# Performance work log

Measured on AMD Instinct MI355X. Metric: run time of the kernel, lower is better.

Reference implementation:

```python
import jax, jax.numpy as jnp
import numpy as np

VOCAB, D, K, B, N = 100000, 512, 256, 4096, 8


def setup_inputs() -> dict:
    key = jax.random.key(0)
    ks = jax.random.split(key, 16)
    inp = {
        'subj_id': jax.random.randint(ks[0], (B, N), 0, VOCAB),
        'subj_w': jax.random.uniform(ks[1], (B, N), dtype=jnp.float32),
        'verb_id': jax.random.randint(ks[2], (B, N), 0, VOCAB),
        'verb_w': jax.random.uniform(ks[3], (B, N), dtype=jnp.float32),
        'obj_id': jax.random.randint(ks[4], (B, N), 0, VOCAB),
        'obj_w': jax.random.uniform(ks[5], (B, N), dtype=jnp.float32),
        'emb': jax.random.normal(ks[6], (VOCAB, D), dtype=jnp.float32) * 0.1,
        't1': jax.random.normal(ks[7], (K, D, D), dtype=jnp.float32) * 0.01,
        't2': jax.random.normal(ks[8], (K, D, D), dtype=jnp.float32) * 0.01,
        't3': jax.random.normal(ks[9], (K, K, K), dtype=jnp.float32) * 0.01,
        'W1': jax.random.normal(ks[10], (K, 2 * D), dtype=jnp.float32) * 0.02,
        'b1': jnp.zeros((K,), dtype=jnp.float32),
        'W2': jax.random.normal(ks[11], (K, 2 * D), dtype=jnp.float32) * 0.02,
        'b2': jnp.zeros((K,), dtype=jnp.float32),
        'W3': jax.random.normal(ks[12], (K, 2 * K), dtype=jnp.float32) * 0.02,
        'b3': jnp.zeros((K,), dtype=jnp.float32),
    }
    return inp


def _phrase_embed(emb, ids, w):
    # (B,N) ids, (B,N) weights -> (B,D) weighted sum of embeddings
    return jnp.einsum('bn,bnd->bd', w, emb[ids])


def _bilinear(t, a, b):
    # t: (k,n1,n2), a: (B,n1), b: (B,n2) -> (B,k)
    return jnp.einsum('kij,bi,bj->bk', t, a, b)


def reference(subj_id, subj_w, verb_id, verb_w, obj_id, obj_w,
              emb, t1, t2, t3, W1, b1, W2, b2, W3, b3):
    subj = _phrase_embed(emb, subj_id, subj_w)
    verb = _phrase_embed(emb, verb_id, verb_w)
    obj = _phrase_embed(emb, obj_id, obj_w)

    r1 = jnp.tanh(_bilinear(t1, subj, verb)
                  + jnp.concatenate([subj, verb], axis=1) @ W1.T + b1)
    r2 = jnp.tanh(_bilinear(t2, verb, obj)
                  + jnp.concatenate([verb, obj], axis=1) @ W2.T + b2)
    r3 = jnp.tanh(_bilinear(t3, r1, r2)
                  + jnp.concatenate([r1, r2], axis=1) @ W3.T + b3)
    return r3
```

## Files before the change

### kernel.cpp

```cpp
#include <hip/hip_runtime.h>
#include <hip/hip_bf16.h>
#include <stdint.h>

typedef __hip_bfloat16 bf16;
typedef __attribute__((ext_vector_type(4))) float f32x4;
typedef __attribute__((ext_vector_type(8))) short bf16x8;

#define K_DIM 256

__device__ __forceinline__ void gl2lds16(const void* g, void* l) {
  __builtin_amdgcn_global_load_lds(
      (const __attribute__((address_space(1))) unsigned int*)g,
      (__attribute__((address_space(3))) unsigned int*)l,
      16, 0, 0);
}

__global__ void embed_kernel(const int* __restrict__ sid, const float* __restrict__ sw,
                             const int* __restrict__ vid, const float* __restrict__ vw,
                             const int* __restrict__ oid, const float* __restrict__ ow,
                             const float* __restrict__ emb,
                             bf16* __restrict__ sv, bf16* __restrict__ vo) {
  int b = blockIdx.x;
  int t = threadIdx.x;
  float s0 = 0.f, s1 = 0.f, v0 = 0.f, v1 = 0.f, o0 = 0.f, o1 = 0.f;
#pragma unroll
  for (int n = 0; n < 8; ++n) {
    int i0 = b * 8 + n;
    { int id = sid[i0]; float w = sw[i0]; const float* r = emb + (size_t)id * 512; s0 += w * r[t]; s1 += w * r[t + 256]; }
    { int id = vid[i0]; float w = vw[i0]; const float* r = emb + (size_t)id * 512; v0 += w * r[t]; v1 += w * r[t + 256]; }
    { int id = oid[i0]; float w = ow[i0]; const float* r = emb + (size_t)id * 512; o0 += w * r[t]; o1 += w * r[t + 256]; }
  }
  size_t base = (size_t)b * 1024;
  bf16 vb0 = __float2bfloat16(v0), vb1 = __float2bfloat16(v1);
  sv[base + t]       = __float2bfloat16(s0);
  sv[base + 256 + t] = __float2bfloat16(s1);
  sv[base + 512 + t] = vb0;
  sv[base + 768 + t] = vb1;
  vo[base + t]       = vb0;
  vo[base + 256 + t] = vb1;
  vo[base + 512 + t] = __float2bfloat16(o0);
  vo[base + 768 + t] = __float2bfloat16(o1);
}

__global__ void cvt_kernel(const float* __restrict__ in, bf16* __restrict__ out, int n) {
  int i = blockIdx.x * blockDim.x + threadIdx.x;
  if (i < n) out[i] = __float2bfloat16(in[i]);
}

__global__ void tcvt_kernel(const float* __restrict__ in, bf16* __restrict__ out, int N) {
  __shared__ float tile[32][33];
  int k = blockIdx.z;
  size_t base = (size_t)k * N * N;
  int j0 = blockIdx.x * 32, i0 = blockIdx.y * 32;
  int tx = threadIdx.x, ty = threadIdx.y;
#pragma unroll
  for (int r = 0; r < 4; ++r)
    tile[ty + 8 * r][tx] = in[base + (size_t)(i0 + ty + 8 * r) * N + j0 + tx];
  __syncthreads();
#pragma unroll
  for (int r = 0; r < 4; ++r)
    out[base + (size_t)(j0 + ty + 8 * r) * N + i0 + tx] = __float2bfloat16(tile[tx][ty + 8 * r]);
}

__global__ __launch_bounds__(256) void lin_kernel(
    const bf16* __restrict__ A, const bf16* __restrict__ W,
    const float* __restrict__ bias, float* __restrict__ Lout, int inner) {
  __shared__ __align__(16) bf16 As[128 * 64];
  __shared__ __align__(16) bf16 Bs[64 * 64];
  int tid = threadIdx.x;
  int wv = tid >> 6, lane = tid & 63;
  int wr = wv >> 1, wc = wv & 1;
  int cl = lane & 15, rg = lane >> 4;
  int r8 = lane >> 3, c8 = lane & 7;
  int cs = c8 ^ r8;
  int b0 = blockIdx.x * 128;
  int n0 = blockIdx.y * 64;
  f32x4 acc[4][2] = {};
  int KO = inner >> 6;
  for (int ko = 0; ko < KO; ++ko) {
    __syncthreads();
#pragma unroll
    for (int it = 0; it < 4; ++it) {
      int m = wv * 32 + it * 8 + r8;
      gl2lds16(A + (size_t)(b0 + m) * inner + ko * 64 + cs * 8, &As[(wv * 32 + it * 8) * 64]);
    }
#pragma unroll
    for (int it = 0; it < 2; ++it) {
      int nn = wv * 16 + it * 8 + r8;
      gl2lds16(W + (size_t)(n0 + nn) * inner + ko * 64 + cs * 8, &Bs[(wv * 16 + it * 8) * 64]);
    }
    __syncthreads();
#pragma unroll
    for (int ks = 0; ks < 2; ++ks) {
      bf16x8 a[4], bb[2];
      int sw = (ks * 4 + rg) ^ (cl & 7);
#pragma unroll
      for (int mt = 0; mt < 4; ++mt) a[mt] = *(const bf16x8*)&As[(wr * 64 + mt * 16 + cl) * 64 + sw * 8];
#pragma unroll
      for (int nt = 0; nt < 2; ++nt) bb[nt] = *(const bf16x8*)&Bs[(wc * 32 + nt * 16 + cl) * 64 + sw * 8];
#pragma unroll
      for (int mt = 0; mt < 4; ++mt)
#pragma unroll
        for (int nt = 0; nt < 2; ++nt)
          acc[mt][nt] = __builtin_amdgcn_mfma_f32_16x16x32_bf16(a[mt], bb[nt], acc[mt][nt], 0, 0, 0);
    }
  }
#pragma unroll
  for (int mt = 0; mt < 4; ++mt)
#pragma unroll
    for (int nt = 0; nt < 2; ++nt) {
      int col = n0 + wc * 32 + nt * 16 + cl;
      float bv = bias[col];
#pragma unroll
      for (int r = 0; r < 4; ++r) {
        int row = b0 + wr * 64 + mt * 16 + rg * 4 + r;
        Lout[(size_t)row * K_DIM + col] = acc[mt][nt][r] + bv;
      }
    }
}

__global__ __launch_bounds__(256) void bilin_kernel(
    const bf16* __restrict__ A, int lda,
    const bf16* __restrict__ T,
    const bf16* __restrict__ V, int ldv, int voff,
    const float* __restrict__ Lm,
    int I, int J,
    bf16* __restrict__ outb, int ldo, int ooff,
    float* __restrict__ outf) {
  __shared__ __align__(16) bf16 As[128 * 64];
  __shared__ __align__(16) bf16 Bs[128 * 64];
  int tid = threadIdx.x;
  int wv = tid >> 6, lane = tid & 63;
  int wr = wv >> 1, wc = wv & 1;
  int cl = lane & 15, rg = lane >> 4;
  int r8 = lane >> 3, c8 = lane & 7;
  int cs = c8 ^ r8;
  int b0 = blockIdx.x * 128;
  int k = blockIdx.y;
  const bf16* Tk = T + (size_t)k * J * I;
  float rsum[16];
#pragma unroll
  for (int v = 0; v < 16; ++v) rsum[v] = 0.f;
  int KO = I >> 6, JB = J >> 7;
  for (int jb = 0; jb < JB; ++jb) {
    f32x4 acc[4][4] = {};
    for (int ko = 0; ko < KO; ++ko) {
      __syncthreads();
#pragma unroll
      for (int it = 0; it < 4; ++it) {
        int m = wv * 32 + it * 8 + r8;
        gl2lds16(A + (size_t)(b0 + m) * lda + ko * 64 + cs * 8, &As[(wv * 32 + it * 8) * 64]);
        gl2lds16(Tk + (size_t)(jb * 128 + m) * I + ko * 64 + cs * 8, &Bs[(wv * 32 + it * 8) * 64]);
      }
      __syncthreads();
#pragma unroll
      for (int ks = 0; ks < 2; ++ks) {
        bf16x8 a[4], bb[4];
        int sw = (ks * 4 + rg) ^ (cl & 7);
#pragma unroll
        for (int mt = 0; mt < 4; ++mt) a[mt] = *(const bf16x8*)&As[(wr * 64 + mt * 16 + cl) * 64 + sw * 8];
#pragma unroll
        for (int nt = 0; nt < 4; ++nt) bb[nt] = *(const bf16x8*)&Bs[(wc * 64 + nt * 16 + cl) * 64 + sw * 8];
#pragma unroll
        for (int mt = 0; mt < 4; ++mt)
#pragma unroll
          for (int nt = 0; nt < 4; ++nt)
            acc[mt][nt] = __builtin_amdgcn_mfma_f32_16x16x32_bf16(a[mt], bb[nt], acc[mt][nt], 0, 0, 0);
      }
    }
#pragma unroll
    for (int mt = 0; mt < 4; ++mt)
#pragma unroll
      for (int r = 0; r < 4; ++r) {
        int gb = b0 + wr * 64 + mt * 16 + rg * 4 + r;
        const bf16* vrow = V + (size_t)gb * ldv + voff + jb * 128 + wc * 64 + cl;
#pragma unroll
        for (int nt = 0; nt < 4; ++nt)
          rsum[mt * 4 + r] += acc[mt][nt][r] * __bfloat162float(vrow[nt * 16]);
      }
  }
#pragma unroll
  for (int v = 0; v < 16; ++v) {
    float x = rsum[v];
    x += __shfl_xor(x, 1);
    x += __shfl_xor(x, 2);
    x += __shfl_xor(x, 4);
    x += __shfl_xor(x, 8);
    rsum[v] = x;
  }
  float* rsum_s = (float*)As;
  __syncthreads();
  if (cl == 0) {
#pragma unroll
    for (int mt = 0; mt < 4; ++mt)
#pragma unroll
      for (int r = 0; r < 4; ++r)
        rsum_s[wc * 128 + wr * 64 + mt * 16 + rg * 4 + r] = rsum[mt * 4 + r];
  }
  __syncthreads();
  if (tid < 128) {
    int gb = b0 + tid;
    float s = rsum_s[tid] + rsum_s[128 + tid] + Lm[(size_t)gb * K_DIM + k];
    float t = tanhf(s);
    if (outb) outb[(size_t)gb * ldo + ooff + k] = __float2bfloat16(t);
    else outf[(size_t)gb * K_DIM + k] = t;
  }
}

extern "C" void kernel_launch(void* const* d_in, const int* in_sizes, int n_in,
                              void* d_out, int out_size, void* d_ws, size_t ws_size,
                              hipStream_t stream) {
  const int*   sid = (const int*)d_in[0];
  const float* sw  = (const float*)d_in[1];
  const int*   vid = (const int*)d_in[2];
  const float* vw  = (const float*)d_in[3];
  const int*   oid = (const int*)d_in[4];
  const float* ow  = (const float*)d_in[5];
  const float* emb = (const float*)d_in[6];
  const float* t1  = (const float*)d_in[7];
  const float* t2  = (const float*)d_in[8];
  const float* t3  = (const float*)d_in[9];
  const float* W1  = (const float*)d_in[10];
  const float* b1  = (const float*)d_in[11];
  const float* W2  = (const float*)d_in[12];
  const float* b2  = (const float*)d_in[13];
  const float* W3  = (const float*)d_in[14];
  const float* b3  = (const float*)d_in[15];

  char* ws = (char*)d_ws;
  bf16*  Tbuf = (bf16*)(ws);
  bf16*  W1b  = (bf16*)(ws + 134217728ull);
  bf16*  W2b  = (bf16*)(ws + 134742016ull);
  bf16*  W3b  = (bf16*)(ws + 135266304ull);
  bf16*  sv   = (bf16*)(ws + 135528448ull);
  bf16*  vo   = (bf16*)(ws + 143917056ull);
  float* Lb   = (float*)(ws + 152305664ull);
  bf16*  r12  = (bf16*)(ws + 156499968ull);

  embed_kernel<<<4096, 256, 0, stream>>>(sid, sw, vid, vw, oid, ow, emb, sv, vo);
  cvt_kernel<<<1024, 256, 0, stream>>>(W1, W1b, 256 * 1024);
  cvt_kernel<<<1024, 256, 0, stream>>>(W2, W2b, 256 * 1024);
  cvt_kernel<<<512, 256, 0, stream>>>(W3, W3b, 256 * 512);

  lin_kernel<<<dim3(32, 4), 256, 0, stream>>>(sv, W1b, b1, Lb, 1024);
  tcvt_kernel<<<dim3(16, 16, 256), dim3(32, 8), 0, stream>>>(t1, Tbuf, 512);
  bilin_kernel<<<dim3(32, 256), 256, 0, stream>>>(sv, 1024, Tbuf, sv, 1024, 512, Lb, 512, 512,
                                                  r12, 512, 0, nullptr);
  lin_kernel<<<dim3(32, 4), 256, 0, stream>>>(vo, W2b, b2, Lb, 1024);
  tcvt_kernel<<<dim3(16, 16, 256), dim3(32, 8), 0, stream>>>(t2, Tbuf, 512);
  bilin_kernel<<<dim3(32, 256), 256, 0, stream>>>(vo, 1024, Tbuf, vo, 1024, 512, Lb, 512, 512,
                                                  r12, 512, 256, nullptr);
  lin_kernel<<<dim3(32, 4), 256, 0, stream>>>(r12, W3b, b3, Lb, 512);
  tcvt_kernel<<<dim3(8, 8, 256), dim3(32, 8), 0, stream>>>(t3, Tbuf, 256);
  bilin_kernel<<<dim3(32, 256), 256, 0, stream>>>(r12, 512, Tbuf, r12, 512, 256, Lb, 256, 256,
                                                  nullptr, 0, 0, (float*)d_out);
}
```

Before: 3.904 ms.

## Use 256x256 tiles with double-buffered LDS prefetch in bilinear kernel

Rewrites the bilinear kernel to use 512-thread blocks that each compute a 256x256 tile, with double-buffered LDS so global-to-LDS loads for the next step run while MFMAs work on the current one. The jb/ko loops are flattened into one pipelined loop, and MFMA sections are raised with setprio. Partial contractions with V are accumulated in a shared scratch array. The larger tile cuts global loads per FLOP and hides load latency, at the cost of more LDS (about 130KB) and more registers, which lowers occupancy.

```diff
diff --git a/kernel.cpp b/kernel.cpp
--- a/kernel.cpp
+++ b/kernel.cpp
@@ -119,91 +119,120 @@
     }
 }
 
-__global__ __launch_bounds__(256) void bilin_kernel(
+__global__ __launch_bounds__(512) void bilin256_kernel(
     const bf16* __restrict__ A, int lda,
     const bf16* __restrict__ T,
     const bf16* __restrict__ V, int ldv, int voff,
     const float* __restrict__ Lm,
-    int I, int J,
+    int I, int J, int koshift,
     bf16* __restrict__ outb, int ldo, int ooff,
     float* __restrict__ outf) {
-  __shared__ __align__(16) bf16 As[128 * 64];
-  __shared__ __align__(16) bf16 Bs[128 * 64];
-  int tid = threadIdx.x;
-  int wv = tid >> 6, lane = tid & 63;
-  int wr = wv >> 1, wc = wv & 1;
-  int cl = lane & 15, rg = lane >> 4;
-  int r8 = lane >> 3, c8 = lane & 7;
-  int cs = c8 ^ r8;
-  int b0 = blockIdx.x * 128;
-  int k = blockIdx.y;
+  __shared__ __align__(16) bf16 As[2][256 * 64];
+  __shared__ __align__(16) bf16 Bs[2][256 * 64];
+  __shared__ float scratch[4][256];
+
+  const int tid  = threadIdx.x;
+  const int wv   = tid >> 6;
+  const int lane = tid & 63;
+  const int wr   = wv >> 2;
+  const int wc   = wv & 3;
+  const int cl   = lane & 15;
+  const int rg   = lane >> 4;
+  const int c8   = lane & 7;
+  const int r8   = lane >> 3;
+  const int cs   = c8 ^ r8;
+  const int b0   = blockIdx.x * 256;
+  const int k    = blockIdx.y;
   const bf16* Tk = T + (size_t)k * J * I;
-  float rsum[16];
-#pragma unroll
-  for (int v = 0; v < 16; ++v) rsum[v] = 0.f;
-  int KO = I >> 6, JB = J >> 7;
-  for (int jb = 0; jb < JB; ++jb) {
-    f32x4 acc[4][4] = {};
-    for (int ko = 0; ko < KO; ++ko) {
-      __syncthreads();
-#pragma unroll
-      for (int it = 0; it < 4; ++it) {
-        int m = wv * 32 + it * 8 + r8;
-        gl2lds16(A + (size_t)(b0 + m) * lda + ko * 64 + cs * 8, &As[(wv * 32 + it * 8) * 64]);
-        gl2lds16(Tk + (size_t)(jb * 128 + m) * I + ko * 64 + cs * 8, &Bs[(wv * 32 + it * 8) * 64]);
+  const int KOm  = (1 << koshift) - 1;
+  const int NT   = (J >> 8) << koshift;
+
+  auto stage_half = [&](int s, int q) {
+    const int db   = s & 1;
+    const int ko_s = s & KOm;
+    const int jb_s = s >> koshift;
+    const int hrow = (q & 1) * 128;
+#pragma unroll
+    for (int p = 0; p < 2; ++p) {
+      const int rloc = hrow + p * 64 + wv * 8 + r8;
+      if (q < 2)
+        gl2lds16(A + (size_t)(b0 + rloc) * lda + ko_s * 64 + cs * 8,
+                 &As[db][(hrow + p * 64 + wv * 8) * 64]);
+      else
+        gl2lds16(Tk + (size_t)(jb_s * 256 + rloc) * I + ko_s * 64 + cs * 8,
+                 &Bs[db][(hrow + p * 64 + wv * 8) * 64]);
+    }
+  };
+
+  const f32x4 zero4 = {0.f, 0.f, 0.f, 0.f};
+  f32x4 acc[8][4];
+
+#pragma unroll
+  for (int q = 0; q < 4; ++q) stage_half(0, q);
+
+  for (int t = 0; t < NT; ++t) {
+    __syncthreads();
+    const int db = t & 1;
+    const int ko = t & KOm;
+    const int jb = t >> koshift;
+    if (ko == 0) {
+#pragma unroll
+      for (int m = 0; m < 8; ++m)
+#pragma unroll
+        for (int n = 0; n < 4; ++n) acc[m][n] = zero4;
+    }
+    const int s = t + 1;
+    const bool hasNext = (s < NT);
+#pragma unroll
+    for (int ph = 0; ph < 2; ++ph) {
+      if (hasNext) { stage_half(s, ph * 2); stage_half(s, ph * 2 + 1); }
+      const int sw = (ph * 4 + rg) ^ c8;
+      bf16x8 a[8], bb[4];
+#pragma unroll
+      for (int mt = 0; mt < 8; ++mt)
+        a[mt] = *(const bf16x8*)&As[db][(wr * 128 + mt * 16 + cl) * 64 + sw * 8];
+#pragma unroll
+      for (int nt = 0; nt < 4; ++nt)
+        bb[nt] = *(const bf16x8*)&Bs[db][(wc * 64 + nt * 16 + cl) * 64 + sw * 8];
+      __builtin_amdgcn_s_setprio(1);
+#pragma unroll
+      for (int mt = 0; mt < 8; ++mt)
+#pragma unroll
+        for (int nt = 0; nt < 4; ++nt)
+          acc[mt][nt] = __builtin_amdgcn_mfma_f32_16x16x32_bf16(a[mt], bb[nt], acc[mt][nt], 0, 0, 0);
+      __builtin_amdgcn_s_setprio(0);
+    }
+    if (ko == KOm) {
+#pragma unroll
+      for (int m = 0; m < 8; ++m) {
+#pragma unroll
+        for (int r = 0; r < 4; ++r) {
+          const int row = wr * 128 + m * 16 + rg * 4 + r;
+          const bf16* vrow = V + (size_t)(b0 + row) * ldv + voff + jb * 256 + wc * 64 + cl;
+          float x = acc[m][0][r] * __bfloat162float(vrow[0])
+                  + acc[m][1][r] * __bfloat162float(vrow[16])
+                  + acc[m][2][r] * __bfloat162float(vrow[32])
+                  + acc[m][3][r] * __bfloat162float(vrow[48]);
+          x += __shfl_xor(x, 1);
+          x += __shfl_xor(x, 2);
+          x += __shfl_xor(x, 4);
+          x += __shfl_xor(x, 8);
+          if (cl == 0) {
+            if (jb == 0) scratch[wc][row] = x;
+            else         scratch[wc][row] += x;
+          }
+        }
       }
-      __syncthreads();
-#pragma unroll
-      for (int ks = 0; ks < 2; ++ks) {
-        bf16x8 a[4], bb[4];
-        int sw = (ks * 4 + rg) ^ (cl & 7);
-#pragma unroll
-        for (int mt = 0; mt < 4; ++mt) a[mt] = *(const bf16x8*)&As[(wr * 64 + mt * 16 + cl) * 64 + sw * 8];
-#pragma unroll
-        for (int nt = 0; nt < 4; ++nt) bb[nt] = *(const bf16x8*)&Bs[(wc * 64 + nt * 16 + cl) * 64 + sw * 8];
-#pragma unroll
-        for (int mt = 0; mt < 4; ++mt)
-#pragma unroll
-          for (int nt = 0; nt < 4; ++nt)
-            acc[mt][nt] = __builtin_amdgcn_mfma_f32_16x16x32_bf16(a[mt], bb[nt], acc[mt][nt], 0, 0, 0);
-      }
-    }
-#pragma unroll
-    for (int mt = 0; mt < 4; ++mt)
-#pragma unroll
-      for (int r = 0; r < 4; ++r) {
-        int gb = b0 + wr * 64 + mt * 16 + rg * 4 + r;
-        const bf16* vrow = V + (size_t)gb * ldv + voff + jb * 128 + wc * 64 + cl;
-#pragma unroll
-        for (int nt = 0; nt < 4; ++nt)
-          rsum[mt * 4 + r] += acc[mt][nt][r] * __bfloat162float(vrow[nt * 16]);
-      }
-  }
-#pragma unroll
-  for (int v = 0; v < 16; ++v) {
-    float x = rsum[v];
-    x += __shfl_xor(x, 1);
-    x += __shfl_xor(x, 2);
-    x += __shfl_xor(x, 4);
-    x += __shfl_xor(x, 8);
-    rsum[v] = x;
-  }
-  float* rsum_s = (float*)As;
+    }
+  }
   __syncthreads();
-  if (cl == 0) {
-#pragma unroll
-    for (int mt = 0; mt < 4; ++mt)
-#pragma unroll
-      for (int r = 0; r < 4; ++r)
-        rsum_s[wc * 128 + wr * 64 + mt * 16 + rg * 4 + r] = rsum[mt * 4 + r];
-  }
-  __syncthreads();
-  if (tid < 128) {
-    int gb = b0 + tid;
-    float s = rsum_s[tid] + rsum_s[128 + tid] + Lm[(size_t)gb * K_DIM + k];
-    float t = tanhf(s);
-    if (outb) outb[(size_t)gb * ldo + ooff + k] = __float2bfloat16(t);
-    else outf[(size_t)gb * K_DIM + k] = t;
+  if (tid < 256) {
+    const int gb = b0 + tid;
+    const float sum = scratch[0][tid] + scratch[1][tid] + scratch[2][tid] + scratch[3][tid]
+                    + Lm[(size_t)gb * K_DIM + k];
+    const float tv = tanhf(sum);
+    if (outb) outb[(size_t)gb * ldo + ooff + k] = __float2bfloat16(tv);
+    else      outf[(size_t)gb * K_DIM + k] = tv;
   }
 }
 
@@ -244,14 +273,14 @@
 
   lin_kernel<<<dim3(32, 4), 256, 0, stream>>>(sv, W1b, b1, Lb, 1024);
   tcvt_kernel<<<dim3(16, 16, 256), dim3(32, 8), 0, stream>>>(t1, Tbuf, 512);
-  bilin_kernel<<<dim3(32, 256), 256, 0, stream>>>(sv, 1024, Tbuf, sv, 1024, 512, Lb, 512, 512,
-                                                  r12, 512, 0, nullptr);
+  bilin256_kernel<<<dim3(16, 256), 512, 0, stream>>>(sv, 1024, Tbuf, sv, 1024, 512, Lb,
+                                                     512, 512, 3, r12, 512, 0, nullptr);
   lin_kernel<<<dim3(32, 4), 256, 0, stream>>>(vo, W2b, b2, Lb, 1024);
   tcvt_kernel<<<dim3(16, 16, 256), dim3(32, 8), 0, stream>>>(t2, Tbuf, 512);
-  bilin_kernel<<<dim3(32, 256), 256, 0, stream>>>(vo, 1024, Tbuf, vo, 1024, 512, Lb, 512, 512,
-                                                  r12, 512, 256, nullptr);
+  bilin256_kernel<<<dim3(16, 256), 512, 0, stream>>>(vo, 1024, Tbuf, vo, 1024, 512, Lb,
+                                                     512, 512, 3, r12, 512, 256, nullptr);
   lin_kernel<<<dim3(32, 4), 256, 0, stream>>>(r12, W3b, b3, Lb, 512);
   tcvt_kernel<<<dim3(8, 8, 256), dim3(32, 8), 0, stream>>>(t3, Tbuf, 256);
-  bilin_kernel<<<dim3(32, 256), 256, 0, stream>>>(r12, 512, Tbuf, r12, 512, 256, Lb, 256, 256,
-                                                  nullptr, 0, 0, (float*)d_out);
-}
+  bilin256_kernel<<<dim3(16, 256), 512, 0, stream>>>(r12, 512, Tbuf, r12, 512, 256, Lb,
+                                                     256, 256, 2, nullptr, 0, 0, (float*)d_out);
+}
```

Result: faster. 3.237 ms (-17.1%).
